# Kernel optimization log

Measured on AMD Instinct MI355X. Metric: run time of the kernel, lower is better.

## Reference

```python
import jax, jax.numpy as jnp
import numpy as np

B, S = 256, 32          # sequence layout for the final (b, s, 1) reshape
BATCH = B * S           # 8192 flattened rows processed per call
IN, U, OUT = 32, 128, 1 # sensory inputs, interneurons, motor outputs
UNFOLDS = 6             # semi-implicit ODE solver unfolds


def _syn_sigmoid(v, mu, sigma):
    # v: [B, P]; mu, sigma: [P, Q] -> [B, P, Q] per-synapse gate
    return jax.nn.sigmoid(sigma * (v[:, :, None] - mu))


def setup_inputs() -> dict:
    key = jax.random.key(0)
    ks = jax.random.split(key, 12)
    inputs = jax.random.normal(ks[0], (BATCH, IN), dtype=jnp.float32)
    state = jax.random.normal(ks[1], (BATCH, U), dtype=jnp.float32)
    # adjacency in {-1, 0, 1} (wiring polarity), baked into W / erev as in _get_variables
    sens_adj = jax.random.randint(ks[2], (IN, U), -1, 2).astype(jnp.float32)
    adj = jax.random.randint(ks[3], (U, U), -1, 2).astype(jnp.float32)
    sensory_mu = jax.random.uniform(ks[4], (IN, U)) * 0.5 + 0.3
    sensory_sigma = jax.random.uniform(ks[5], (IN, U)) * 5.0 + 3.0
    # NOTE: original applies +w_init_min OUTSIDE the |adj| mask; reproduced faithfully
    sensory_W = jnp.abs(sens_adj) * jax.random.uniform(ks[6], (IN, U)) * 0.9 + 0.1
    sensory_erev = sens_adj  # erev_init_factor = 1
    mu = jax.random.uniform(ks[7], (U, U)) * 0.5 + 0.3
    sigma = jax.random.uniform(ks[8], (U, U)) * 5.0 + 3.0
    W = jnp.abs(adj) * jax.random.uniform(ks[9], (U, U)) * 0.9 + 0.1
    erev = adj
    vleak = jax.random.uniform(ks[10], (U,)) * 0.4 - 0.2
    gleak = jnp.ones((U,), jnp.float32)        # gleak_init_min == gleak_init_max == 1
    cm_t = jnp.ones((U,), jnp.float32) * 0.5    # cm_init_min == cm_init_max == 0.5
    in_w = jnp.ones((IN,), jnp.float32)         # affine input mapping (init ones/zeros)
    in_b = jnp.zeros((IN,), jnp.float32)
    out_w = jnp.ones((OUT,), jnp.float32)       # affine output mapping
    out_b = jnp.zeros((OUT,), jnp.float32)
    return dict(inputs=inputs, state=state, sensory_mu=sensory_mu,
                sensory_sigma=sensory_sigma, sensory_W=sensory_W,
                sensory_erev=sensory_erev, mu=mu, sigma=sigma, W=W, erev=erev,
                vleak=vleak, gleak=gleak, cm_t=cm_t, in_w=in_w, in_b=in_b,
                out_w=out_w, out_b=out_b, b=B, s=S)


def reference(inputs, state, sensory_mu, sensory_sigma, sensory_W, sensory_erev,
              mu, sigma, W, erev, vleak, gleak, cm_t, in_w, in_b, out_w, out_b,
              b, s):
    x = inputs * in_w + in_b                                   # _map_inputs (Affine)
    # sensory synapse activations, computed once: [BATCH, IN, U]
    sa = sensory_W * _syn_sigmoid(x, sensory_mu, sensory_sigma)
    w_num_s = jnp.sum(sa * sensory_erev, axis=1)               # [BATCH, U]
    w_den_s = jnp.sum(sa, axis=1)                              # [BATCH, U]

    def step(v, _):
        wa = W * _syn_sigmoid(v, mu, sigma)                    # [BATCH, U, U]
        w_num = jnp.sum(wa * erev, axis=1) + w_num_s
        w_den = jnp.sum(wa, axis=1) + w_den_s
        v_new = (cm_t * v + gleak * vleak + w_num) / (cm_t + gleak + w_den)
        return v_new, None

    v, _ = jax.lax.scan(step, state, None, length=UNFOLDS)
    outputs = (v[:, :OUT] * out_w + out_b).reshape(b, s, 1)    # _map_outputs
    return outputs, v
```

## Files before the change

kernel.cpp:

```cpp
#include <hip/hip_runtime.h>

#define NIN 32
#define NU  128
#define RPB 16
#define RPT 8
#define UNFOLDS 6
#define LOG2E 1.44269504088896340736f

typedef float float4v __attribute__((ext_vector_type(4)));

#define SPN (NIN * NU)
#define RPN (NU * NU)

__global__ void pack_params(const float* __restrict__ mu,
                            const float* __restrict__ sig,
                            const float* __restrict__ W,
                            const float* __restrict__ erev,
                            float4v* __restrict__ out, int n) {
    int idx = blockIdx.x * blockDim.x + threadIdx.x;
    if (idx < n) {
        float sg = sig[idx];
        float s2 = -LOG2E * sg;
        float sm2 = -s2 * mu[idx];
        float Wv = W[idx];
        float We = Wv * erev[idx];
        out[idx] = (float4v){s2, sm2, We, Wv};
    }
}

__global__ __launch_bounds__(256, 2)
void wormnet_main(const float* __restrict__ inputs,
                  const float* __restrict__ state,
                  const float4v* __restrict__ sp,
                  const float4v* __restrict__ rp,
                  const float* __restrict__ vleak,
                  const float* __restrict__ gleak,
                  const float* __restrict__ cm_t,
                  const float* __restrict__ in_w, const float* __restrict__ in_b,
                  const float* __restrict__ out_w, const float* __restrict__ out_b,
                  float* __restrict__ out_y,
                  float* __restrict__ out_v)
{
    __shared__ __align__(16) float xs[NIN * RPB];
    __shared__ __align__(16) float vs[2][NU * RPB];

    const int tid  = threadIdx.x;
    const int j    = tid & (NU - 1);
    const int rh   = tid >> 7;
    const int r0   = rh * RPT;
    const int base = blockIdx.x * RPB;

    {
        int i = tid & (NIN - 1);
        int r = tid >> 5;
        xs[i * RPB + r]     = inputs[(base + r) * NIN + i] * in_w[i] + in_b[i];
        xs[i * RPB + r + 8] = inputs[(base + r + 8) * NIN + i] * in_w[i] + in_b[i];
    }
    {
        #pragma unroll
        for (int r = 0; r < RPT; ++r) {
            vs[0][j * RPB + r0 + r] = state[(base + r0 + r) * NU + j];
        }
    }
    __syncthreads();

    float numS[RPT], denS[RPT];
    #pragma unroll
    for (int r = 0; r < RPT; ++r) { numS[r] = 0.0f; denS[r] = 0.0f; }

    {
        const float4v* pp = sp + j;
        #pragma unroll 2
        for (int i = 0; i < NIN; ++i) {
            float4v p = pp[0]; pp += NU;
            float4v xa = *(const float4v*)&xs[i * RPB + r0];
            float4v xb = *(const float4v*)&xs[i * RPB + r0 + 4];
            float a[RPT];
            #pragma unroll
            for (int r = 0; r < 4; ++r) {
                a[r]     = 1.0f + __builtin_amdgcn_exp2f(__builtin_fmaf(p.x, xa[r], p.y));
                a[r + 4] = 1.0f + __builtin_amdgcn_exp2f(__builtin_fmaf(p.x, xb[r], p.y));
            }
            #pragma unroll
            for (int q = 0; q < RPT / 2; ++q) {
                float rq = __builtin_amdgcn_rcpf(a[2*q] * a[2*q+1]);
                float s0 = rq * a[2*q+1];
                float s1 = rq * a[2*q];
                numS[2*q]   = __builtin_fmaf(p.z, s0, numS[2*q]);
                denS[2*q]   = __builtin_fmaf(p.w, s0, denS[2*q]);
                numS[2*q+1] = __builtin_fmaf(p.z, s1, numS[2*q+1]);
                denS[2*q+1] = __builtin_fmaf(p.w, s1, denS[2*q+1]);
            }
        }
    }

    const float cm = cm_t[j];
    const float gl = gleak[j];
    const float glvl = gl * vleak[j];
    const float cg = cm + gl;
    float vold[RPT];
    #pragma unroll
    for (int r = 0; r < RPT; ++r) vold[r] = vs[0][j * RPB + r0 + r];

    int cur = 0;
    for (int u = 0; u < UNFOLDS; ++u) {
        float num[RPT], den[RPT];
        #pragma unroll
        for (int r = 0; r < RPT; ++r) { num[r] = numS[r]; den[r] = denS[r]; }

        const float4v* pp = rp + j;
        #pragma unroll 2
        for (int i = 0; i < NU; ++i) {
            float4v p = pp[0]; pp += NU;
            float4v va = *(const float4v*)&vs[cur][i * RPB + r0];
            float4v vb = *(const float4v*)&vs[cur][i * RPB + r0 + 4];
            float a[RPT];
            #pragma unroll
            for (int r = 0; r < 4; ++r) {
                a[r]     = 1.0f + __builtin_amdgcn_exp2f(__builtin_fmaf(p.x, va[r], p.y));
                a[r + 4] = 1.0f + __builtin_amdgcn_exp2f(__builtin_fmaf(p.x, vb[r], p.y));
            }
            #pragma unroll
            for (int q = 0; q < RPT / 2; ++q) {
                float rq = __builtin_amdgcn_rcpf(a[2*q] * a[2*q+1]);
                float s0 = rq * a[2*q+1];
                float s1 = rq * a[2*q];
                num[2*q]   = __builtin_fmaf(p.z, s0, num[2*q]);
                den[2*q]   = __builtin_fmaf(p.w, s0, den[2*q]);
                num[2*q+1] = __builtin_fmaf(p.z, s1, num[2*q+1]);
                den[2*q+1] = __builtin_fmaf(p.w, s1, den[2*q+1]);
            }
        }

        #pragma unroll
        for (int r = 0; r < RPT; ++r) {
            float tn = __builtin_fmaf(cm, vold[r], glvl) + num[r];
            float td = cg + den[r];
            float vn = tn * __builtin_amdgcn_rcpf(td);
            vold[r] = vn;
            vs[cur ^ 1][j * RPB + r0 + r] = vn;
        }
        __syncthreads();
        cur ^= 1;
    }

    #pragma unroll
    for (int r = 0; r < RPT; ++r) {
        out_v[(base + r0 + r) * NU + j] = vold[r];
    }
    if (j == 0) {
        const float ow = out_w[0], ob = out_b[0];
        #pragma unroll
        for (int r = 0; r < RPT; ++r) {
            out_y[base + r0 + r] = __builtin_fmaf(vold[r], ow, ob);
        }
    }
}

extern "C" void kernel_launch(void* const* d_in, const int* in_sizes, int n_in,
                              void* d_out, int out_size, void* d_ws, size_t ws_size,
                              hipStream_t stream) {
    const float* inputs  = (const float*)d_in[0];
    const float* state   = (const float*)d_in[1];
    const float* smu     = (const float*)d_in[2];
    const float* ssig    = (const float*)d_in[3];
    const float* sW      = (const float*)d_in[4];
    const float* serev   = (const float*)d_in[5];
    const float* rmu     = (const float*)d_in[6];
    const float* rsig    = (const float*)d_in[7];
    const float* rW      = (const float*)d_in[8];
    const float* rerev   = (const float*)d_in[9];
    const float* vleak   = (const float*)d_in[10];
    const float* gleak   = (const float*)d_in[11];
    const float* cm_t    = (const float*)d_in[12];
    const float* in_w    = (const float*)d_in[13];
    const float* in_b    = (const float*)d_in[14];
    const float* out_w   = (const float*)d_in[15];
    const float* out_b   = (const float*)d_in[16];

    const int batch = in_sizes[1] / NU;
    float* out_y = (float*)d_out;
    float* out_v = (float*)d_out + batch;

    float4v* sp = (float4v*)d_ws;
    float4v* rp = sp + SPN;

    hipLaunchKernelGGL(pack_params, dim3((SPN + 255) / 256), dim3(256), 0, stream,
                       smu, ssig, sW, serev, sp, SPN);
    hipLaunchKernelGGL(pack_params, dim3((RPN + 255) / 256), dim3(256), 0, stream,
                       rmu, rsig, rW, rerev, rp, RPN);

    dim3 grid(batch / RPB), block(256);
    hipLaunchKernelGGL(wormnet_main, grid, block, 0, stream,
                       inputs, state, sp, rp,
                       vleak, gleak, cm_t, in_w, in_b, out_w, out_b,
                       out_y, out_v);
}
```

Measured before the change: 277.3 us.

## Split synapse reduction across four thread groups with shared-memory combine

Each block now handles 8 rows with 512 threads. Four groups of 128 threads each reduce a quarter of the presynaptic (and sensory) neurons for all 8 rows. Partial numerator and denominator sums are combined through shared memory before each state update. This multiplies the number of resident waves to hide exp/rcp and load latency, since the old 16-row, 256-thread layout left only a few waves per CU. The cost is an extra shared-memory reduction and a second barrier per unfold, plus more shared memory per block.

Result: faster. 267.6 us (-3.5%).

```diff
diff --git a/kernel.cpp b/kernel.cpp
--- a/kernel.cpp
+++ b/kernel.cpp
@@ -2,8 +2,8 @@
 
 #define NIN 32
 #define NU  128
-#define RPB 16
-#define RPT 8
+#define RPB 8
+#define NQ  4
 #define UNFOLDS 6
 #define LOG2E 1.44269504088896340736f
 
@@ -28,7 +28,7 @@
     }
 }
 
-__global__ __launch_bounds__(256, 2)
+__global__ __launch_bounds__(512, 8)
 void wormnet_main(const float* __restrict__ inputs,
                   const float* __restrict__ state,
                   const float4v* __restrict__ sp,
@@ -42,54 +42,56 @@
                   float* __restrict__ out_v)
 {
     __shared__ __align__(16) float xs[NIN * RPB];
-    __shared__ __align__(16) float vs[2][NU * RPB];
+    __shared__ __align__(16) float vs[NU * RPB];
+    __shared__ float rn[RPB][NQ][NU];
+    __shared__ float rd[RPB][NQ][NU];
 
     const int tid  = threadIdx.x;
     const int j    = tid & (NU - 1);
-    const int rh   = tid >> 7;
-    const int r0   = rh * RPT;
+    const int q    = tid >> 7;
     const int base = blockIdx.x * RPB;
-
-    {
+    const int u0   = q * 2;
+
+    if (tid < NIN * RPB) {
         int i = tid & (NIN - 1);
         int r = tid >> 5;
-        xs[i * RPB + r]     = inputs[(base + r) * NIN + i] * in_w[i] + in_b[i];
-        xs[i * RPB + r + 8] = inputs[(base + r + 8) * NIN + i] * in_w[i] + in_b[i];
-    }
+        xs[i * RPB + r] = inputs[(base + r) * NIN + i] * in_w[i] + in_b[i];
+    }
+    float vold[2];
+    #pragma unroll
+    for (int k = 0; k < 2; ++k) {
+        float v = state[(base + u0 + k) * NU + j];
+        vold[k] = v;
+        vs[j * RPB + u0 + k] = v;
+    }
+    __syncthreads();
+
+    float numS[RPB], denS[RPB];
+    #pragma unroll
+    for (int r = 0; r < RPB; ++r) { numS[r] = 0.0f; denS[r] = 0.0f; }
     {
-        #pragma unroll
-        for (int r = 0; r < RPT; ++r) {
-            vs[0][j * RPB + r0 + r] = state[(base + r0 + r) * NU + j];
-        }
-    }
-    __syncthreads();
-
-    float numS[RPT], denS[RPT];
-    #pragma unroll
-    for (int r = 0; r < RPT; ++r) { numS[r] = 0.0f; denS[r] = 0.0f; }
-
-    {
-        const float4v* pp = sp + j;
+        const float4v* pp = sp + q * (NIN / NQ) * NU + j;
         #pragma unroll 2
-        for (int i = 0; i < NIN; ++i) {
+        for (int ii = 0; ii < NIN / NQ; ++ii) {
+            const int i = q * (NIN / NQ) + ii;
             float4v p = pp[0]; pp += NU;
-            float4v xa = *(const float4v*)&xs[i * RPB + r0];
-            float4v xb = *(const float4v*)&xs[i * RPB + r0 + 4];
-            float a[RPT];
+            float4v xa = *(const float4v*)&xs[i * RPB];
+            float4v xb = *(const float4v*)&xs[i * RPB + 4];
+            float a[RPB];
             #pragma unroll
             for (int r = 0; r < 4; ++r) {
                 a[r]     = 1.0f + __builtin_amdgcn_exp2f(__builtin_fmaf(p.x, xa[r], p.y));
                 a[r + 4] = 1.0f + __builtin_amdgcn_exp2f(__builtin_fmaf(p.x, xb[r], p.y));
             }
             #pragma unroll
-            for (int q = 0; q < RPT / 2; ++q) {
-                float rq = __builtin_amdgcn_rcpf(a[2*q] * a[2*q+1]);
-                float s0 = rq * a[2*q+1];
-                float s1 = rq * a[2*q];
-                numS[2*q]   = __builtin_fmaf(p.z, s0, numS[2*q]);
-                denS[2*q]   = __builtin_fmaf(p.w, s0, denS[2*q]);
-                numS[2*q+1] = __builtin_fmaf(p.z, s1, numS[2*q+1]);
-                denS[2*q+1] = __builtin_fmaf(p.w, s1, denS[2*q+1]);
+            for (int w = 0; w < RPB / 2; ++w) {
+                float rq = __builtin_amdgcn_rcpf(a[2*w] * a[2*w+1]);
+                float s0 = rq * a[2*w+1];
+                float s1 = rq * a[2*w];
+                numS[2*w]   = __builtin_fmaf(p.z, s0, numS[2*w]);
+                denS[2*w]   = __builtin_fmaf(p.w, s0, denS[2*w]);
+                numS[2*w+1] = __builtin_fmaf(p.z, s1, numS[2*w+1]);
+                denS[2*w+1] = __builtin_fmaf(p.w, s1, denS[2*w+1]);
             }
         }
     }
@@ -98,61 +100,66 @@
     const float gl = gleak[j];
     const float glvl = gl * vleak[j];
     const float cg = cm + gl;
-    float vold[RPT];
-    #pragma unroll
-    for (int r = 0; r < RPT; ++r) vold[r] = vs[0][j * RPB + r0 + r];
-
-    int cur = 0;
+
     for (int u = 0; u < UNFOLDS; ++u) {
-        float num[RPT], den[RPT];
-        #pragma unroll
-        for (int r = 0; r < RPT; ++r) { num[r] = numS[r]; den[r] = denS[r]; }
-
-        const float4v* pp = rp + j;
+        float num[RPB], den[RPB];
+        #pragma unroll
+        for (int r = 0; r < RPB; ++r) { num[r] = numS[r]; den[r] = denS[r]; }
+
+        const float4v* pp = rp + q * (NU / NQ) * NU + j;
         #pragma unroll 2
-        for (int i = 0; i < NU; ++i) {
+        for (int ii = 0; ii < NU / NQ; ++ii) {
+            const int i = q * (NU / NQ) + ii;
             float4v p = pp[0]; pp += NU;
-            float4v va = *(const float4v*)&vs[cur][i * RPB + r0];
-            float4v vb = *(const float4v*)&vs[cur][i * RPB + r0 + 4];
-            float a[RPT];
+            float4v va = *(const float4v*)&vs[i * RPB];
+            float4v vb = *(const float4v*)&vs[i * RPB + 4];
+            float a[RPB];
             #pragma unroll
             for (int r = 0; r < 4; ++r) {
                 a[r]     = 1.0f + __builtin_amdgcn_exp2f(__builtin_fmaf(p.x, va[r], p.y));
                 a[r + 4] = 1.0f + __builtin_amdgcn_exp2f(__builtin_fmaf(p.x, vb[r], p.y));
             }
             #pragma unroll
-            for (int q = 0; q < RPT / 2; ++q) {
-                float rq = __builtin_amdgcn_rcpf(a[2*q] * a[2*q+1]);
-                float s0 = rq * a[2*q+1];
-                float s1 = rq * a[2*q];
-                num[2*q]   = __builtin_fmaf(p.z, s0, num[2*q]);
-                den[2*q]   = __builtin_fmaf(p.w, s0, den[2*q]);
-                num[2*q+1] = __builtin_fmaf(p.z, s1, num[2*q+1]);
-                den[2*q+1] = __builtin_fmaf(p.w, s1, den[2*q+1]);
-            }
-        }
-
-        #pragma unroll
-        for (int r = 0; r < RPT; ++r) {
-            float tn = __builtin_fmaf(cm, vold[r], glvl) + num[r];
-            float td = cg + den[r];
-            float vn = tn * __builtin_amdgcn_rcpf(td);
-            vold[r] = vn;
-            vs[cur ^ 1][j * RPB + r0 + r] = vn;
+            for (int w = 0; w < RPB / 2; ++w) {
+                float rq = __builtin_amdgcn_rcpf(a[2*w] * a[2*w+1]);
+                float s0 = rq * a[2*w+1];
+                float s1 = rq * a[2*w];
+                num[2*w]   = __builtin_fmaf(p.z, s0, num[2*w]);
+                den[2*w]   = __builtin_fmaf(p.w, s0, den[2*w]);
+                num[2*w+1] = __builtin_fmaf(p.z, s1, num[2*w+1]);
+                den[2*w+1] = __builtin_fmaf(p.w, s1, den[2*w+1]);
+            }
+        }
+
+        #pragma unroll
+        for (int r = 0; r < RPB; ++r) {
+            rn[r][q][j] = num[r];
+            rd[r][q][j] = den[r];
         }
         __syncthreads();
-        cur ^= 1;
+
+        #pragma unroll
+        for (int k = 0; k < 2; ++k) {
+            const int r = u0 + k;
+            float tn = rn[r][0][j] + rn[r][1][j] + rn[r][2][j] + rn[r][3][j];
+            float td = rd[r][0][j] + rd[r][1][j] + rd[r][2][j] + rd[r][3][j];
+            float vn = (__builtin_fmaf(cm, vold[k], glvl) + tn)
+                       * __builtin_amdgcn_rcpf(cg + td);
+            vold[k] = vn;
+            vs[j * RPB + r] = vn;
+        }
+        __syncthreads();
     }
 
     #pragma unroll
-    for (int r = 0; r < RPT; ++r) {
-        out_v[(base + r0 + r) * NU + j] = vold[r];
+    for (int k = 0; k < 2; ++k) {
+        out_v[(base + u0 + k) * NU + j] = vold[k];
     }
     if (j == 0) {
         const float ow = out_w[0], ob = out_b[0];
         #pragma unroll
-        for (int r = 0; r < RPT; ++r) {
-            out_y[base + r0 + r] = __builtin_fmaf(vold[r], ow, ob);
+        for (int k = 0; k < 2; ++k) {
+            out_y[base + u0 + k] = __builtin_fmaf(vold[k], ow, ob);
         }
     }
 }
@@ -190,7 +197,7 @@
     hipLaunchKernelGGL(pack_params, dim3((RPN + 255) / 256), dim3(256), 0, stream,
                        rmu, rsig, rW, rerev, rp, RPN);
 
-    dim3 grid(batch / RPB), block(256);
+    dim3 grid(batch / RPB), block(NU * NQ);
     hipLaunchKernelGGL(wormnet_main, grid, block, 0, stream,
                        inputs, state, sp, rp,
                        vleak, gleak, cm_t, in_w, in_b, out_w, out_b,
```
